# Performance work log

Hardware: AMD Instinct MI355X
Metric: run time of the kernel (lower is better)

The kernel has to match this reference:

```python
import jax
import jax.numpy as jnp
import numpy as np

# ---- static config (mirrors ReduceMask.__init__ / get_block_params) ----
N, H, W = 32, 1024, 1024
BH, BW = 16, 16            # block_size (pool window)
KH, KW = 3, 3              # kernel_size
SH, SW = 1, 1              # stride
PH, PW = KH // 2, KW // 2  # symmetric padding = 1,1
BSH, BSW = BH - KH + SH, BW - KW + SW   # block_stride = 14,14
BCH = (H + 2 * PH - BH) // BSH + 1      # block_cnt h = 73
BCW = (W + 2 * PW - BW) // BSW + 1      # block_cnt w = 73
THRESHOLD = 0.9
TOTAL = N * BCH * BCW      # fixed upper bound on number of active blocks


def setup_inputs() -> dict:
    key = jax.random.key(0)
    mask = jax.random.uniform(key, (N, 1, H, W), dtype=jnp.float32)
    return {"mask": mask}


def reference(mask):
    # pad H,W by kernel_size//2 (constant zeros), as in F.pad(mask, padding)
    x = jnp.pad(mask, ((0, 0), (0, 0), (PH, PH), (PW, PW)))
    # max_pool2d with window=block_size, stride=block_stride, padding=0
    pooled = jax.lax.reduce_window(
        x, -jnp.inf, jax.lax.max,
        window_dimensions=(1, 1, BH, BW),
        window_strides=(1, 1, BSH, BSW),
        padding='VALID',
    )[:, 0]  # squeeze channel -> [N, BCH, BCW]
    active = pooled > THRESHOLD
    # torch.nonzero -> row-major (n, bh, bw) indices; fixed-size padded with -1 for jit
    nz = jnp.nonzero(active, size=TOTAL, fill_value=-1)
    return jnp.stack(nz, axis=1).astype(jnp.int32)  # [TOTAL, 3]
```

## Files before the change

### kernel.cpp

```cpp
#include <hip/hip_runtime.h>

#define NI    32
#define HH    1024
#define WW    1024
#define BHW   16
#define BS    14
#define NBH   73
#define NBW   73
#define NCHUNK (NI * NBH)
#define TOTAL  (NI * NBH * NBW)
#define ROWDW  (3 * NBW)

struct umask2 { unsigned long long x, y; };

__device__ __forceinline__ float4 max4(float4 a, float4 b) {
    return make_float4(fmaxf(a.x, b.x), fmaxf(a.y, b.y),
                       fmaxf(a.z, b.z), fmaxf(a.w, b.w));
}

__device__ __forceinline__ void write_full_row(int* __restrict__ out,
                                               int chunk, int n, int by, int tid) {
    if (tid < ROWDW) {
        const int q = tid / 3;
        const int comp = tid - 3 * q;
        out[(size_t)chunk * ROWDW + tid] = (comp == 0) ? n : ((comp == 1) ? by : q);
    }
}

__global__ __launch_bounds__(256, 8) void pool_kernel(const float* __restrict__ mask,
                                                      umask2* __restrict__ masks,
                                                      int* __restrict__ counts,
                                                      int* __restrict__ deficit,
                                                      int* __restrict__ out) {
    const int chunk = blockIdx.x;
    const int n  = chunk / NBH;
    const int by = chunk % NBH;
    const int tid  = threadIdx.x;
    const int lane = tid & 63;
    const int wave = tid >> 6;

    __shared__ float colmax[WW];
    __shared__ unsigned long long wb[4];
    __shared__ unsigned long long sm0, sm1;

    const int r0 = by * BS - 1;
    const int rs = max(r0, 0);
    const int nr = (by > 0) ? 16 : 15;
    const float* p = mask + (size_t)n * HH * WW + (size_t)rs * WW + tid * 4;

    const float4 a0 = *(const float4*)(p + 0 * (size_t)WW);
    const float4 a1 = *(const float4*)(p + 1 * (size_t)WW);
    const float4 a2 = *(const float4*)(p + 2 * (size_t)WW);
    const float4 a3 = *(const float4*)(p + 3 * (size_t)WW);
    const float4 a4 = *(const float4*)(p + 4 * (size_t)WW);
    const float4 a5 = *(const float4*)(p + 5 * (size_t)WW);
    float4 m = max4(max4(max4(a0, a1), max4(a2, a3)), max4(a4, a5));

    const float mm = fmaxf(fmaxf(m.x, m.y), fmaxf(m.z, m.w));
    const unsigned long long bal = __ballot(mm > 0.9f);
    if (lane == 0) wb[wave] = bal;
    __syncthreads();

    bool whit = true;
    if (tid < NBW) {
        const int c0 = tid * BS;
        const int lo = (c0 + 2) >> 2;
        const int hi = (c0 + 11) >> 2;
        const int w0 = lo >> 6, sh = lo & 63;
        unsigned long long bits = wb[w0] >> sh;
        if (w0 < 3 && sh) bits |= wb[w0 + 1] << (64 - sh);
        const int nb = hi - lo + 1;
        whit = (bits & ((1ull << nb) - 1ull)) != 0ull;
    }
    const bool done = __syncthreads_and((int)whit) != 0;

    if (done) {
        if (tid == 0) {
            umask2 mk; mk.x = ~0ull; mk.y = (1ull << (NBW - 64)) - 1ull;
            masks[chunk] = mk;
            counts[chunk] = NBW;
        }
        write_full_row(out, chunk, n, by, tid);
        return;
    }

    for (int r = 6; r < nr; ++r)
        m = max4(m, *(const float4*)(p + (size_t)r * WW));

    const int c = tid * 4;
    colmax[c + 0] = m.x;
    colmax[c + 1] = m.y;
    colmax[c + 2] = m.z;
    colmax[c + 3] = m.w;
    __syncthreads();

    int f = 0;
    if (tid < NBW) {
        const int c0 = tid * BS - 1;
        float mx = colmax[max(c0, 0)];
        #pragma unroll
        for (int dc = 1; dc < BHW; ++dc) mx = fmaxf(mx, colmax[c0 + dc]);
        f = (mx > 0.9f) ? 1 : 0;
    }
    const unsigned long long b = __ballot(f);
    if (wave == 0 && lane == 0) sm0 = b;
    if (wave == 1 && lane == 0) sm1 = b;
    __syncthreads();

    const int cnt = __popcll(sm0) + __popcll(sm1);
    if (tid == 0) {
        umask2 mk; mk.x = sm0; mk.y = sm1;
        masks[chunk] = mk;
        counts[chunk] = cnt;
        if (cnt != NBW) atomicAdd(deficit, 1);
    }
    if (cnt == NBW)
        write_full_row(out, chunk, n, by, tid);
}

__global__ __launch_bounds__(128) void scatter_kernel(const umask2* __restrict__ masks,
                                                      const int* __restrict__ counts,
                                                      const int* __restrict__ deficit,
                                                      int* __restrict__ out) {
    if (*deficit == 0) return;

    const int chunk = blockIdx.x;
    const int n  = chunk / NBH;
    const int by = chunk % NBH;
    const int tid  = threadIdx.x;
    const int lane = tid & 63;
    const int wave = tid >> 6;

    __shared__ int wsum[2];

    int partial = 0;
    for (int i = tid; i < chunk; i += 128) partial += counts[i];
    #pragma unroll
    for (int off = 32; off > 0; off >>= 1) partial += __shfl_down(partial, off, 64);
    if (lane == 0) wsum[wave] = partial;

    const umask2 m = masks[chunk];
    __syncthreads();
    const int e = wsum[0] + wsum[1];
    const int c = __popcll(m.x) + __popcll(m.y);

    if (tid < NBW) {
        int f, prefix;
        if (wave == 0) {
            f = (int)((m.x >> tid) & 1ull);
            prefix = __popcll(m.x & ((1ull << tid) - 1ull));
        } else {
            const int t = tid - 64;
            f = (int)((m.y >> t) & 1ull);
            prefix = __popcll(m.x) + __popcll(m.y & ((1ull << t) - 1ull));
        }
        if (f) {
            const int pos = e + prefix;
            out[3 * pos + 0] = n;
            out[3 * pos + 1] = by;
            out[3 * pos + 2] = tid;
        }
    }

    const int slack = NBW - c;
    if (slack > 0) {
        const int s_incl = (chunk + 1) * NBW - (e + c);
        const int base3 = 3 * (TOTAL - s_incl);
        const int n3 = 3 * slack;
        for (int i = tid; i < n3; i += 128) out[base3 + i] = -1;
    }
}

extern "C" void kernel_launch(void* const* d_in, const int* in_sizes, int n_in,
                              void* d_out, int out_size, void* d_ws, size_t ws_size,
                              hipStream_t stream) {
    const float* mask = (const float*)d_in[0];
    int* out = (int*)d_out;

    umask2* masks = (umask2*)d_ws;
    int* counts = (int*)(masks + NCHUNK);
    int* deficit = counts + NCHUNK;

    hipMemsetAsync(deficit, 0, sizeof(int), stream);
    pool_kernel<<<NCHUNK, 256, 0, stream>>>(mask, masks, counts, deficit, out);
    scatter_kernel<<<NCHUNK, 128, 0, stream>>>(masks, counts, deficit, out);
}
```

Baseline: 179.9 us.

## Fuse scatter into pool kernel via last-block ticket fallback

Removes the separate scatter kernel launch. Each pool block takes an atomic ticket after a threadfence, and the last block to finish checks whether every row was full. If not, it serially compacts all chunk masks into the output and pads the rest with -1. This saves one kernel launch in the common case where all rows are full. The rare partial case becomes a single-block serial loop over 2336 chunks, which would be much slower if it ever ran.

```diff
diff --git a/kernel.cpp b/kernel.cpp
--- a/kernel.cpp
+++ b/kernel.cpp
@@ -23,14 +23,16 @@
     if (tid < ROWDW) {
         const int q = tid / 3;
         const int comp = tid - 3 * q;
-        out[(size_t)chunk * ROWDW + tid] = (comp == 0) ? n : ((comp == 1) ? by : q);
+        int v;
+        if (comp == 0) v = n; else if (comp == 1) v = by; else v = q;
+        out[(size_t)chunk * ROWDW + tid] = v;
     }
 }
 
 __global__ __launch_bounds__(256, 8) void pool_kernel(const float* __restrict__ mask,
                                                       umask2* __restrict__ masks,
                                                       int* __restrict__ counts,
-                                                      int* __restrict__ deficit,
+                                                      int* __restrict__ done_ctr,
                                                       int* __restrict__ out) {
     const int chunk = blockIdx.x;
     const int n  = chunk / NBH;
@@ -42,6 +44,8 @@
     __shared__ float colmax[WW];
     __shared__ unsigned long long wb[4];
     __shared__ unsigned long long sm0, sm1;
+    __shared__ int slast;
+    __shared__ int s_e;
 
     const int r0 = by * BS - 1;
     const int rs = max(r0, 0);
@@ -81,94 +85,89 @@
             counts[chunk] = NBW;
         }
         write_full_row(out, chunk, n, by, tid);
-        return;
+    } else {
+        for (int r = 6; r < nr; ++r)
+            m = max4(m, *(const float4*)(p + (size_t)r * WW));
+
+        const int c = tid * 4;
+        colmax[c + 0] = m.x;
+        colmax[c + 1] = m.y;
+        colmax[c + 2] = m.z;
+        colmax[c + 3] = m.w;
+        __syncthreads();
+
+        int f = 0;
+        if (tid < NBW) {
+            const int c0 = tid * BS - 1;
+            float mx = colmax[max(c0, 0)];
+            #pragma unroll
+            for (int dc = 1; dc < BHW; ++dc) mx = fmaxf(mx, colmax[c0 + dc]);
+            f = (mx > 0.9f) ? 1 : 0;
+        }
+        const unsigned long long b = __ballot(f);
+        if (wave == 0 && lane == 0) sm0 = b;
+        if (wave == 1 && lane == 0) sm1 = b;
+        __syncthreads();
+
+        const int cnt = __popcll(sm0) + __popcll(sm1);
+        if (tid == 0) {
+            umask2 mk; mk.x = sm0; mk.y = sm1;
+            masks[chunk] = mk;
+            counts[chunk] = cnt;
+        }
+        if (cnt == NBW)
+            write_full_row(out, chunk, n, by, tid);
     }
 
-    for (int r = 6; r < nr; ++r)
-        m = max4(m, *(const float4*)(p + (size_t)r * WW));
+    __threadfence();
+    if (tid == 0) {
+        const int ticket = atomicAdd(done_ctr, 1);
+        slast = (ticket == NCHUNK - 1) ? 1 : 0;
+    }
+    __syncthreads();
+    if (!slast) return;
 
-    const int c = tid * 4;
-    colmax[c + 0] = m.x;
-    colmax[c + 1] = m.y;
-    colmax[c + 2] = m.z;
-    colmax[c + 3] = m.w;
-    __syncthreads();
-
-    int f = 0;
-    if (tid < NBW) {
-        const int c0 = tid * BS - 1;
-        float mx = colmax[max(c0, 0)];
-        #pragma unroll
-        for (int dc = 1; dc < BHW; ++dc) mx = fmaxf(mx, colmax[c0 + dc]);
-        f = (mx > 0.9f) ? 1 : 0;
-    }
-    const unsigned long long b = __ballot(f);
-    if (wave == 0 && lane == 0) sm0 = b;
-    if (wave == 1 && lane == 0) sm1 = b;
-    __syncthreads();
-
-    const int cnt = __popcll(sm0) + __popcll(sm1);
-    if (tid == 0) {
-        umask2 mk; mk.x = sm0; mk.y = sm1;
-        masks[chunk] = mk;
-        counts[chunk] = cnt;
-        if (cnt != NBW) atomicAdd(deficit, 1);
-    }
-    if (cnt == NBW)
-        write_full_row(out, chunk, n, by, tid);
-}
-
-__global__ __launch_bounds__(128) void scatter_kernel(const umask2* __restrict__ masks,
-                                                      const int* __restrict__ counts,
-                                                      const int* __restrict__ deficit,
-                                                      int* __restrict__ out) {
-    if (*deficit == 0) return;
-
-    const int chunk = blockIdx.x;
-    const int n  = chunk / NBH;
-    const int by = chunk % NBH;
-    const int tid  = threadIdx.x;
-    const int lane = tid & 63;
-    const int wave = tid >> 6;
-
-    __shared__ int wsum[2];
-
+    __threadfence();
     int partial = 0;
-    for (int i = tid; i < chunk; i += 128) partial += counts[i];
+    for (int i = tid; i < NCHUNK; i += 256) partial += counts[i];
     #pragma unroll
     for (int off = 32; off > 0; off >>= 1) partial += __shfl_down(partial, off, 64);
+    __shared__ int wsum[4];
     if (lane == 0) wsum[wave] = partial;
+    __syncthreads();
+    const int grand = wsum[0] + wsum[1] + wsum[2] + wsum[3];
+    if (grand == TOTAL) return;
 
-    const umask2 m = masks[chunk];
+    if (tid == 0) s_e = 0;
     __syncthreads();
-    const int e = wsum[0] + wsum[1];
-    const int c = __popcll(m.x) + __popcll(m.y);
-
-    if (tid < NBW) {
-        int f, prefix;
-        if (wave == 0) {
-            f = (int)((m.x >> tid) & 1ull);
-            prefix = __popcll(m.x & ((1ull << tid) - 1ull));
-        } else {
-            const int t = tid - 64;
-            f = (int)((m.y >> t) & 1ull);
-            prefix = __popcll(m.x) + __popcll(m.y & ((1ull << t) - 1ull));
+    for (int ch = 0; ch < NCHUNK; ++ch) {
+        const umask2 mk = masks[ch];
+        const int cn  = ch / NBH;
+        const int cby = ch % NBH;
+        const int e = s_e;
+        if (tid < NBW) {
+            int f, prefix;
+            if (tid < 64) {
+                f = (int)((mk.x >> tid) & 1ull);
+                prefix = __popcll(mk.x & ((1ull << tid) - 1ull));
+            } else {
+                const int t = tid - 64;
+                f = (int)((mk.y >> t) & 1ull);
+                prefix = __popcll(mk.x) + __popcll(mk.y & ((1ull << t) - 1ull));
+            }
+            if (f) {
+                const int pos = e + prefix;
+                out[3 * pos + 0] = cn;
+                out[3 * pos + 1] = cby;
+                out[3 * pos + 2] = tid;
+            }
         }
-        if (f) {
-            const int pos = e + prefix;
-            out[3 * pos + 0] = n;
-            out[3 * pos + 1] = by;
-            out[3 * pos + 2] = tid;
-        }
+        __syncthreads();
+        if (tid == 0) s_e = e + __popcll(mk.x) + __popcll(mk.y);
+        __syncthreads();
     }
-
-    const int slack = NBW - c;
-    if (slack > 0) {
-        const int s_incl = (chunk + 1) * NBW - (e + c);
-        const int base3 = 3 * (TOTAL - s_incl);
-        const int n3 = 3 * slack;
-        for (int i = tid; i < n3; i += 128) out[base3 + i] = -1;
-    }
+    const int gt = s_e;
+    for (int i = 3 * gt + tid; i < 3 * TOTAL; i += 256) out[i] = -1;
 }
 
 extern "C" void kernel_launch(void* const* d_in, const int* in_sizes, int n_in,
@@ -179,9 +178,8 @@
 
     umask2* masks = (umask2*)d_ws;
     int* counts = (int*)(masks + NCHUNK);
-    int* deficit = counts + NCHUNK;
+    int* done_ctr = counts + NCHUNK;
 
-    hipMemsetAsync(deficit, 0, sizeof(int), stream);
-    pool_kernel<<<NCHUNK, 256, 0, stream>>>(mask, masks, counts, deficit, out);
-    scatter_kernel<<<NCHUNK, 128, 0, stream>>>(masks, counts, deficit, out);
+    (void)hipMemsetAsync(done_ctr, 0, sizeof(int), stream);
+    pool_kernel<<<NCHUNK, 256, 0, stream>>>(mask, masks, counts, done_ctr, out);
 }
```

Result: slower. 488.8 us (+171.7%).
